# Performance work log

Hardware: AMD Instinct MI355X
Metric: run time of the kernel (lower is better)

Reference implementation:

```python
import jax, jax.numpy as jnp
import numpy as np

S, HID, H, KV, D = 2048, 3584, 16, 8, 256
WINDOW = 1024
SOFTCAP = 50.0
SCALING = 256 ** (-0.5)  # query_pre_attn_scalar ** -0.5
EPS = 1e-6
ROPE_THETA = 10000.0


def _rope_tables(seq_len, dim, theta):
    inv_freq = 1.0 / (theta ** (np.arange(0, dim, 2, dtype=np.float32) / dim))
    t = np.arange(seq_len, dtype=np.float32)
    freqs = np.outer(t, inv_freq)            # [S, D/2]
    emb = np.concatenate([freqs, freqs], -1)  # [S, D]
    return jnp.asarray(np.cos(emb)), jnp.asarray(np.sin(emb))


def setup_inputs() -> dict:
    key = jax.random.key(0)
    ks = jax.random.split(key, 3)
    hidden_states = jax.random.normal(ks[0], (S, HID), jnp.float32)
    w_qkv = jax.random.normal(ks[1], (HID, (H + 2 * KV) * D), jnp.float32) * (HID ** -0.5)
    w_o = jax.random.normal(ks[2], (H * D, HID), jnp.float32) * ((H * D) ** -0.5)
    q_norm_w = jnp.zeros((D,), jnp.float32)  # gemma norm stores weight as (1 + w)
    k_norm_w = jnp.zeros((D,), jnp.float32)
    cos, sin = _rope_tables(S, D, ROPE_THETA)
    return {"hidden_states": hidden_states, "w_qkv": w_qkv, "w_o": w_o,
            "q_norm_w": q_norm_w, "k_norm_w": k_norm_w, "cos": cos, "sin": sin}


def _rms_norm(x, w):
    # gemma-style: fp32 norm, scale by (1 + w); x: [S, h, D]
    xf = x.astype(jnp.float32)
    var = jnp.mean(xf * xf, axis=-1, keepdims=True)
    return (xf * jax.lax.rsqrt(var + EPS) * (1.0 + w)).astype(x.dtype)


def _rotate_half(x):
    x1, x2 = jnp.split(x, 2, axis=-1)
    return jnp.concatenate([-x2, x1], axis=-1)


def _apply_rope(x, cos, sin):
    # x: [S, h, D]; cos/sin: [S, D]
    c = cos[:, None, :]
    s = sin[:, None, :]
    return x * c + _rotate_half(x) * s


def reference(hidden_states, w_qkv, w_o, q_norm_w, k_norm_w, cos, sin):
    qkv = hidden_states @ w_qkv                      # [S, (H+2KV)*D]
    q = qkv[:, : H * D].reshape(S, H, D)
    k = qkv[:, H * D: (H + KV) * D].reshape(S, KV, D)
    v = qkv[:, (H + KV) * D:].reshape(S, KV, D)

    q = _rms_norm(q, q_norm_w)                       # gemma3 q_norm
    k = _rms_norm(k, k_norm_w)                       # gemma3 k_norm
    q = _apply_rope(q, cos, sin)
    k = _apply_rope(k, cos, sin)

    # GQA: expand KV heads to H
    rep = H // KV
    k = jnp.repeat(k, rep, axis=1)                   # [S, H, D]
    v = jnp.repeat(v, rep, axis=1)

    scores = jnp.einsum('shd,thd->hst', q, k) * SCALING  # [H, S, S]
    scores = SOFTCAP * jnp.tanh(scores / SOFTCAP)        # logit softcapping

    i = jnp.arange(S)[:, None]
    j = jnp.arange(S)[None, :]
    allowed = (j <= i) & ((i - j) < WINDOW)              # causal + sliding window
    scores = jnp.where(allowed[None], scores, jnp.float32(-1e30))

    attn = jax.nn.softmax(scores, axis=-1)
    out = jnp.einsum('hst,thd->shd', attn, v).reshape(S, H * D)
    return out @ w_o                                     # [S, HID]
```

## Files before the change

kernel.cpp:

```cpp
#include <hip/hip_runtime.h>
#include <hip/hip_bf16.h>
#include <math.h>

typedef __attribute__((ext_vector_type(8))) short short8;
typedef __attribute__((ext_vector_type(4))) float floatx4;
typedef unsigned short u16;

typedef __attribute__((address_space(1))) const void* gas_ptr;
typedef __attribute__((address_space(3))) void* las_ptr;

__device__ __forceinline__ float bf2f(u16 h) {
  union { unsigned u; float f; } v; v.u = ((unsigned)h) << 16; return v.f;
}
__device__ __forceinline__ u16 f2bf(float f) {
  union { float f; unsigned u; } v; v.f = f;
  unsigned r = v.u + 0x7FFFu + ((v.u >> 16) & 1u);
  return (u16)(r >> 16);
}
__device__ __forceinline__ float ldf_dyn(const void* p, size_t i, bool f32) {
  return f32 ? ((const float*)p)[i] : bf2f(((const u16*)p)[i]);
}
__device__ __forceinline__ short8 load8_dyn(const void* p, size_t idx, bool f32) {
  if (f32) {
    const float* f = (const float*)p;
    float4 a = *(const float4*)(f + idx);
    float4 b = *(const float4*)(f + idx + 4);
    short8 r;
    r[0] = (short)f2bf(a.x); r[1] = (short)f2bf(a.y);
    r[2] = (short)f2bf(a.z); r[3] = (short)f2bf(a.w);
    r[4] = (short)f2bf(b.x); r[5] = (short)f2bf(b.y);
    r[6] = (short)f2bf(b.z); r[7] = (short)f2bf(b.w);
    return r;
  }
  return *(const short8*)((const u16*)p + idx);
}
__device__ __forceinline__ void gl_lds16(const u16* g, u16* l) {
  __builtin_amdgcn_global_load_lds((gas_ptr)g, (las_ptr)l, 16, 0, 0);
}

__global__ void probe_dtype_kernel(const void* hidden, int* flag) {
  __shared__ int cnt;
  if (threadIdx.x == 0) cnt = 0;
  __syncthreads();
  const u16* h = (const u16*)hidden;
  int local = 0;
  for (int i = threadIdx.x; i < 8192; i += 256) {
    u16 u = h[i];
    int e = (u >> 7) & 0xFF;
    if ((e >= 64 && e <= 160) || (u & 0x7FFF) == 0) local++;
  }
  atomicAdd(&cnt, local);
  __syncthreads();
  if (threadIdx.x == 0) *flag = (cnt < 7700) ? 1 : 0;
}

__global__ __launch_bounds__(256) void convert_dyn_kernel(
    const void* __restrict__ src, u16* __restrict__ dst, size_t n,
    const int* __restrict__ flagp)
{
  const bool f32 = (*flagp != 0);
  size_t i = ((size_t)blockIdx.x * 256 + threadIdx.x) * 8;
  if (i < n) *(short8*)(dst + i) = load8_dyn(src, i, f32);
}

__global__ __launch_bounds__(256) void transpose_dyn_kernel(
    const void* __restrict__ src, u16* __restrict__ dst, int R, int C,
    const int* __restrict__ flagp)
{
  const bool f32 = (*flagp != 0);
  const int c0 = blockIdx.x * 64, r0 = blockIdx.y * 64;
  __shared__ __attribute__((aligned(16))) u16 T[64][72];
  const int tid = threadIdx.x;
#pragma unroll
  for (int i = 0; i < 2; i++) {
    int t = tid + i * 256;
    int r = t >> 3, cc = (t & 7) << 3;
    *(short8*)(&T[r][cc]) = load8_dyn(src, (size_t)(r0 + r) * C + c0 + cc, f32);
  }
  __syncthreads();
#pragma unroll
  for (int i = 0; i < 2; i++) {
    int t = tid + i * 256;
    int cr = t >> 3, rc = (t & 7) << 3;
    __attribute__((aligned(16))) u16 tmp[8];
#pragma unroll
    for (int j = 0; j < 8; j++) tmp[j] = T[rc + j][cr];
    *(short8*)(dst + (size_t)(c0 + cr) * R + r0 + rc) = *(const short8*)tmp;
  }
}

#define BAR() __builtin_amdgcn_s_barrier()
#define SCB() __builtin_amdgcn_sched_barrier(0)
#define LGKM0() do { asm volatile("s_waitcnt lgkmcnt(0)" ::: "memory"); SCB(); } while (0)
#define VMW(n) do { asm volatile("s_waitcnt vmcnt(" #n ")" ::: "memory"); SCB(); } while (0)

#define STG_AU(s, u, t) \
  gl_lds16(pa + (size_t)((u) * 64) * K + (size_t)(t) * 64, \
           ldsw + (s) * 32768 + (u) * 4096)
#define STG_BU(s, u, t) \
  gl_lds16(pb + (size_t)((u) * 64) * K + (size_t)(t) * 64, \
           ldsw + (s) * 32768 + 16384 + (u) * 4096)

#define RD_FA(s, miH) do { \
  _Pragma("unroll") \
  for (int m2 = 0; m2 < 4; m2++) { \
    const u16* _r = LDS + (s) * 32768 + wm * 8192 + (miH) * 4096 + m2 * 1024 + lane15 * 64; \
    fa[m2][0] = *(const short8*)(_r + colA0); \
    fa[m2][1] = *(const short8*)(_r + colA1); \
  } \
} while (0)
#define RD_FB(s, niH) do { \
  _Pragma("unroll") \
  for (int n2 = 0; n2 < 2; n2++) { \
    const u16* _r = LDS + (s) * 32768 + 16384 + wn * 4096 + (niH) * 2048 + n2 * 1024 + lane15 * 64; \
    fb[niH][n2][0] = *(const short8*)(_r + colA0); \
    fb[niH][n2][1] = *(const short8*)(_r + colA1); \
  } \
} while (0)
#define MFMA_Q(miH, niH) do { \
  __builtin_amdgcn_s_setprio(1); \
  _Pragma("unroll") \
  for (int m2 = 0; m2 < 4; m2++) \
    _Pragma("unroll") \
    for (int n2 = 0; n2 < 2; n2++) { \
      acc[(miH) * 4 + m2][(niH) * 2 + n2] = __builtin_amdgcn_mfma_f32_16x16x32_bf16( \
          fa[m2][0], fb[niH][n2][0], acc[(miH) * 4 + m2][(niH) * 2 + n2], 0, 0, 0); \
      acc[(miH) * 4 + m2][(niH) * 2 + n2] = __builtin_amdgcn_mfma_f32_16x16x32_bf16( \
          fa[m2][1], fb[niH][n2][1], acc[(miH) * 4 + m2][(niH) * 2 + n2], 0, 0, 0); \
    } \
  __builtin_amdgcn_s_setprio(0); \
  SCB(); \
} while (0)

__global__ __launch_bounds__(512, 2) void gemm8p_kernel(
    const u16* __restrict__ A, const u16* __restrict__ BT, u16* __restrict__ C,
    int M, int N, int K)
{
  __shared__ __attribute__((aligned(16))) u16 LDS[65536];
  const int tid = threadIdx.x;
  const int wave = tid >> 6, lane = tid & 63;
  const int lane15 = lane & 15, quad = lane >> 4;
  const int wm = wave >> 2, wn = wave & 3;
  const int m0 = blockIdx.y * 256, n0 = blockIdx.x * 256;

  const int rloc = wave * 8 + (lane >> 3);
  const int sxor = lane >> 3;
  const int csw = ((lane & 7) ^ sxor) * 8;
  const u16* pa = A + (size_t)(m0 + rloc) * K + csw;
  const u16* pb = BT + (size_t)(n0 + rloc) * K + csw;
  u16* ldsw = LDS + wave * 512;

  const int swz = lane15 & 7;
  const int colA0 = (quad ^ swz) * 8;
  const int colA1 = ((4 + quad) ^ swz) * 8;

  floatx4 acc[8][4];
#pragma unroll
  for (int i = 0; i < 8; i++)
#pragma unroll
    for (int j = 0; j < 4; j++) acc[i][j] = (floatx4){0.f, 0.f, 0.f, 0.f};
  short8 fa[4][2], fb[2][2][2];

  const int NT = K >> 6, NI = NT >> 1;

  STG_AU(0, 0, 0); STG_AU(0, 2, 0);
  STG_BU(0, 0, 0); STG_BU(0, 1, 0);
  STG_BU(0, 2, 0); STG_BU(0, 3, 0);
  STG_AU(0, 1, 0); STG_AU(0, 3, 0);
  STG_AU(1, 0, 1); STG_AU(1, 2, 1);
  STG_BU(1, 0, 1); STG_BU(1, 1, 1);
  STG_BU(1, 2, 1); STG_BU(1, 3, 1);
  VMW(8);
  BAR();

  for (int i = 0; i < NI - 1; i++) {
    const int t1 = 2 * i + 1, t2 = 2 * i + 2, t3 = 2 * i + 3;
    RD_FA(0, 0); RD_FB(0, 0);
    STG_AU(1, 1, t1); STG_AU(1, 3, t1);
    BAR(); LGKM0(); MFMA_Q(0, 0); BAR();
    RD_FB(0, 1);
    STG_AU(0, 0, t2); STG_AU(0, 2, t2);
    BAR(); LGKM0(); MFMA_Q(0, 1); VMW(10); BAR();
    RD_FA(0, 1);
    STG_BU(0, 0, t2); STG_BU(0, 1, t2);
    BAR(); LGKM0(); MFMA_Q(1, 1); BAR();
    STG_BU(0, 2, t2); STG_BU(0, 3, t2);
    BAR(); MFMA_Q(1, 0); VMW(8); BAR();
    RD_FA(1, 0); RD_FB(1, 0);
    STG_AU(0, 1, t2); STG_AU(0, 3, t2);
    BAR(); LGKM0(); MFMA_Q(0, 0); BAR();
    RD_FB(1, 1);
    STG_AU(1, 0, t3); STG_AU(1, 2, t3);
    BAR(); LGKM0(); MFMA_Q(0, 1); VMW(10); BAR();
    RD_FA(1, 1);
    STG_BU(1, 0, t3); STG_BU(1, 1, t3);
    BAR(); LGKM0(); MFMA_Q(1, 1); BAR();
    STG_BU(1, 2, t3); STG_BU(1, 3, t3);
    BAR(); MFMA_Q(1, 0); VMW(8); BAR();
  }

  {
    const int tL = NT - 1;
    RD_FA(0, 0); RD_FB(0, 0);
    STG_AU(1, 1, tL); STG_AU(1, 3, tL);
    BAR(); LGKM0(); MFMA_Q(0, 0); BAR();
    RD_FB(0, 1);
    BAR(); LGKM0(); MFMA_Q(0, 1); VMW(8); BAR();
    RD_FA(0, 1);
    BAR(); LGKM0(); MFMA_Q(1, 1); BAR();
    BAR(); MFMA_Q(1, 0); VMW(2); BAR();
    RD_FA(1, 0); RD_FB(1, 0);
    BAR(); LGKM0(); MFMA_Q(0, 0); BAR();
    RD_FB(1, 1);
    BAR(); LGKM0(); MFMA_Q(0, 1); VMW(0); BAR();
    RD_FA(1, 1);
    BAR(); LGKM0(); MFMA_Q(1, 1); BAR();
    BAR(); MFMA_Q(1, 0);
  }

#pragma unroll
  for (int mi = 0; mi < 8; mi++)
#pragma unroll
    for (int rr = 0; rr < 4; rr++) {
      int m = m0 + wm * 128 + mi * 16 + quad * 4 + rr;
      u16* crow = C + (size_t)m * N + n0 + wn * 64;
#pragma unroll
      for (int ni = 0; ni < 4; ni++) crow[ni * 16 + lane15] = f2bf(acc[mi][ni][rr]);
    }
}

#define NSTG_A(s, u, t) \
  gl_lds16(pa + (size_t)((u) * 64) * K + (size_t)(t) * 64, \
           ldsw + (s) * 24576 + (u) * 4096)
#define NSTG_B(s, u, t) \
  gl_lds16(pb + (size_t)((u) * 64) * K + (size_t)(t) * 64, \
           ldsw + (s) * 24576 + 8192 + (u) * 4096)

#define NRD_FA(s, miH) do { \
  _Pragma("unroll") \
  for (int m2 = 0; m2 < 2; m2++) { \
    const u16* _r = LDS + (s) * 24576 + wm * 4096 + (miH) * 2048 + m2 * 1024 + lane15 * 64; \
    fa[m2][0] = *(const short8*)(_r + colA0); \
    fa[m2][1] = *(const short8*)(_r + colA1); \
  } \
} while (0)
#define NRD_FB(s, niH) do { \
  _Pragma("unroll") \
  for (int n2 = 0; n2 < 2; n2++) { \
    const u16* _r = LDS + (s) * 24576 + 8192 + wn * 4096 + (niH) * 2048 + n2 * 1024 + lane15 * 64; \
    fb[niH][n2][0] = *(const short8*)(_r + colA0); \
    fb[niH][n2][1] = *(const short8*)(_r + colA1); \
  } \
} while (0)
#define NMFMA_Q(miH, niH) do { \
  __builtin_amdgcn_s_setprio(1); \
  _Pragma("unroll") \
  for (int m2 = 0; m2 < 2; m2++) \
    _Pragma("unroll") \
    for (int n2 = 0; n2 < 2; n2++) { \
      acc[(miH) * 2 + m2][(niH) * 2 + n2] = __builtin_amdgcn_mfma_f32_16x16x32_bf16( \
          fa[m2][0], fb[niH][n2][0], acc[(miH) * 2 + m2][(niH) * 2 + n2], 0, 0, 0); \
      acc[(miH) * 2 + m2][(niH) * 2 + n2] = __builtin_amdgcn_mfma_f32_16x16x32_bf16( \
          fa[m2][1], fb[niH][n2][1], acc[(miH) * 2 + m2][(niH) * 2 + n2], 0, 0, 0); \
    } \
  __builtin_amdgcn_s_setprio(0); \
  SCB(); \
} while (0)

__global__ __launch_bounds__(512, 2) void gemm8pn_kernel(
    const u16* __restrict__ A, const u16* __restrict__ BT, void* __restrict__ C,
    int M, int N, int K, const int* __restrict__ flagp, int cdyn)
{
  __shared__ __attribute__((aligned(16))) u16 LDS[49152];
  const int tid = threadIdx.x;
  const int wave = tid >> 6, lane = tid & 63;
  const int lane15 = lane & 15, quad = lane >> 4;
  const int wm = wave >> 2, wn = wave & 3;
  const int m0 = blockIdx.y * 128, n0 = blockIdx.x * 256;

  const int rloc = wave * 8 + (lane >> 3);
  const int sxor = lane >> 3;
  const int csw = ((lane & 7) ^ sxor) * 8;
  const u16* pa = A + (size_t)(m0 + rloc) * K + csw;
  const u16* pb = BT + (size_t)(n0 + rloc) * K + csw;
  u16* ldsw = LDS + wave * 512;

  const int swz = lane15 & 7;
  const int colA0 = (quad ^ swz) * 8;
  const int colA1 = ((4 + quad) ^ swz) * 8;

  floatx4 acc[4][4];
#pragma unroll
  for (int i = 0; i < 4; i++)
#pragma unroll
    for (int j = 0; j < 4; j++) acc[i][j] = (floatx4){0.f, 0.f, 0.f, 0.f};
  short8 fa[2][2], fb[2][2][2];

  const int NT = K >> 6, NI = NT >> 1;

  NSTG_B(0, 0, 0); NSTG_B(0, 1, 0); NSTG_B(0, 2, 0); NSTG_B(0, 3, 0);
  NSTG_A(0, 0, 0); NSTG_A(0, 1, 0);
  NSTG_B(1, 0, 1); NSTG_B(1, 1, 1); NSTG_B(1, 2, 1); NSTG_B(1, 3, 1);
  NSTG_A(1, 0, 1); NSTG_A(1, 1, 1);
  VMW(6);
  BAR();

  for (int i = 0; i < NI - 1; i++) {
    const int t2 = 2 * i + 2, t3 = 2 * i + 3;
    NRD_FA(0, 0); NRD_FB(0, 0);
    BAR(); LGKM0(); NMFMA_Q(0, 0); BAR();
    NRD_FB(0, 1);
    BAR(); LGKM0(); NMFMA_Q(0, 1); BAR();
    NRD_FA(0, 1);
    NSTG_B(0, 0, t2); NSTG_B(0, 1, t2);
    BAR(); LGKM0(); NMFMA_Q(1, 1); BAR();
    NSTG_B(0, 2, t2); NSTG_B(0, 3, t2); NSTG_A(0, 0, t2); NSTG_A(0, 1, t2);
    BAR(); NMFMA_Q(1, 0); VMW(6); BAR();
    NRD_FA(1, 0); NRD_FB(1, 0);
    BAR(); LGKM0(); NMFMA_Q(0, 0); BAR();
    NRD_FB(1, 1);
    BAR(); LGKM0(); NMFMA_Q(0, 1); BAR();
    NRD_FA(1, 1);
    NSTG_B(1, 0, t3); NSTG_B(1, 1, t3);
    BAR(); LGKM0(); NMFMA_Q(1, 1); BAR();
    NSTG_B(1, 2, t3); NSTG_B(1, 3, t3); NSTG_A(1, 0, t3); NSTG_A(1, 1, t3);
    BAR(); NMFMA_Q(1, 0); VMW(6); BAR();
  }

  {
    NRD_FA(0, 0); NRD_FB(0, 0);
    BAR(); LGKM0(); NMFMA_Q(0, 0); BAR();
    NRD_FB(0, 1);
    BAR(); LGKM0(); NMFMA_Q(0, 1); BAR();
    NRD_FA(0, 1);
    BAR(); LGKM0(); NMFMA_Q(1, 1); BAR();
    BAR(); NMFMA_Q(1, 0); VMW(0); BAR();
    NRD_FA(1, 0); NRD_FB(1, 0);
    BAR(); LGKM0(); NMFMA_Q(0, 0); BAR();
    NRD_FB(1, 1);
    BAR(); LGKM0(); NMFMA_Q(0, 1); BAR();
    NRD_FA(1, 1);
    BAR(); LGKM0(); NMFMA_Q(1, 1); BAR();
    NMFMA_Q(1, 0);
  }

  const bool cf32 = cdyn && (*flagp != 0);
  if (cf32) {
    float* Cf = (float*)C;
#pragma unroll
    for (int mi = 0; mi < 4; mi++)
#pragma unroll
      for (int rr = 0; rr < 4; rr++) {
        int m = m0 + wm * 64 + mi * 16 + quad * 4 + rr;
        float* crow = Cf + (size_t)m * N + n0 + wn * 64;
#pragma unroll
        for (int ni = 0; ni < 4; ni++) crow[ni * 16 + lane15] = acc[mi][ni][rr];
      }
  } else {
    u16* Cb = (u16*)C;
#pragma unroll
    for (int mi = 0; mi < 4; mi++)
#pragma unroll
      for (int rr = 0; rr < 4; rr++) {
        int m = m0 + wm * 64 + mi * 16 + quad * 4 + rr;
        u16* crow = Cb + (size_t)m * N + n0 + wn * 64;
#pragma unroll
        for (int ni = 0; ni < 4; ni++) crow[ni * 16 + lane15] = f2bf(acc[mi][ni][rr]);
      }
  }
}

__global__ __launch_bounds__(256) void normrope_kernel(
    u16* __restrict__ qkv, const void* __restrict__ qw,
    const void* __restrict__ kw, const void* __restrict__ cosb,
    const void* __restrict__ sinb, const int* __restrict__ flagp)
{
  const bool f32 = (*flagp != 0);
  const int s = blockIdx.x;
  const int wave = threadIdx.x >> 6, lane = threadIdx.x & 63;
  const int hh = blockIdx.y * 4 + wave;
  const int col = (hh < 16) ? hh * 256 : 4096 + (hh - 16) * 256;
  const void* w = (hh < 16) ? qw : kw;
  u16* row = qkv + (size_t)s * 8192 + col;

  float x[4];
#pragma unroll
  for (int j = 0; j < 4; j++) x[j] = bf2f(row[lane + j * 64]);

  float ss = x[0] * x[0] + x[1] * x[1] + x[2] * x[2] + x[3] * x[3];
#pragma unroll
  for (int off = 32; off > 0; off >>= 1) ss += __shfl_xor(ss, off);
  float inv = rsqrtf(ss * (1.0f / 256.0f) + 1e-6f);

  float y[4];
#pragma unroll
  for (int j = 0; j < 4; j++)
    y[j] = x[j] * inv * (1.0f + ldf_dyn(w, lane + j * 64, f32));
  float rot[4] = {-y[2], -y[3], y[0], y[1]};
#pragma unroll
  for (int j = 0; j < 4; j++) {
    int d = lane + j * 64;
    float c = ldf_dyn(cosb, (size_t)s * 256 + d, f32);
    float sn = ldf_dyn(sinb, (size_t)s * 256 + d, f32);
    row[d] = f2bf(y[j] * c + rot[j] * sn);
  }
}

__global__ __launch_bounds__(256) void vtrans_kernel(
    const u16* __restrict__ qkv, u16* __restrict__ vT)
{
  const int s0 = blockIdx.x * 64, d0 = blockIdx.y * 64, kv = blockIdx.z;
  __shared__ __attribute__((aligned(16))) u16 T[64][72];
  const int tid = threadIdx.x;
#pragma unroll
  for (int i = 0; i < 2; i++) {
    int c = tid + i * 256;
    int r = c >> 3, dc = (c & 7) << 3;
    *(short8*)(&T[r][dc]) =
        *(const short8*)(qkv + (size_t)(s0 + r) * 8192 + 6144 + kv * 256 + d0 + dc);
  }
  __syncthreads();
#pragma unroll
  for (int i = 0; i < 2; i++) {
    int c = tid + i * 256;
    int dr = c >> 3, sc = (c & 7) << 3;
    __attribute__((aligned(16))) u16 tmp[8];
#pragma unroll
    for (int j = 0; j < 8; j++) tmp[j] = T[sc + j][dr];
    *(short8*)(vT + (size_t)kv * 524288 + (size_t)(d0 + dr) * 2048 + s0 + sc) =
        *(const short8*)tmp;
  }
}

__global__ __launch_bounds__(256) void attn_kernel(
    const u16* __restrict__ qkv, const u16* __restrict__ vT,
    u16* __restrict__ aout)
{
  const int h = blockIdx.y, kvh = h >> 1;
  const int q0 = blockIdx.x * 64;
  const int tid = threadIdx.x;
  const int wave = tid >> 6, lane = tid & 63;
  const int lane15 = lane & 15, quad = lane >> 4;

  __shared__ __attribute__((aligned(16))) u16 Ks[64 * 264];
  __shared__ __attribute__((aligned(16))) u16 Vs[256 * 72];
  __shared__ __attribute__((aligned(16))) u16 Ps[4][16 * 72];

  short8 aq[8];
  const u16* qrow = qkv + (size_t)(q0 + wave * 16 + lane15) * 8192 + h * 256;
#pragma unroll
  for (int kt = 0; kt < 8; kt++)
    aq[kt] = *(const short8*)(qrow + kt * 32 + quad * 8);

  floatx4 zero = {0.0f, 0.0f, 0.0f, 0.0f};
  floatx4 accO[16];
#pragma unroll
  for (int i = 0; i < 16; i++) accO[i] = zero;
  float lR[4] = {0.0f, 0.0f, 0.0f, 0.0f};

  const int iRow = q0 + wave * 16 + quad * 4;
  const int kb_lo = (q0 >= 1023) ? ((q0 - 1023) >> 6) : 0;
  const int kb_hi = q0 >> 6;

  for (int kb = kb_lo; kb <= kb_hi; kb++) {
    const int t0 = kb << 6;
#pragma unroll
    for (int i = 0; i < 8; i++) {
      int c = tid + i * 256;
      int r = c >> 5, dc = (c & 31) << 3;
      *(short8*)(&Ks[r * 264 + dc]) =
          *(const short8*)(qkv + (size_t)(t0 + r) * 8192 + 4096 + kvh * 256 + dc);
    }
#pragma unroll
    for (int i = 0; i < 8; i++) {
      int c = tid + i * 256;
      int dr = c >> 3, tc = (c & 7) << 3;
      *(short8*)(&Vs[dr * 72 + tc]) =
          *(const short8*)(vT + (size_t)kvh * 524288 + (size_t)dr * 2048 + t0 + tc);
    }
    __syncthreads();

    const int relHi = q0 + 16 * wave + 15 - t0;
    const int relLo = q0 + 16 * wave - 1023 - t0;
    const int niHiR = relHi >> 4;
    const int niHi = (niHiR > 3) ? 3 : niHiR;
    int niLo = relLo >> 4; if (niLo < 0) niLo = 0;
    const int ktHiR = relHi >> 5;
    const int ktHi = (ktHiR > 1) ? 1 : ktHiR;
    int ktLo = relLo >> 5; if (ktLo < 0) ktLo = 0;

    float pv[4][4];
#pragma unroll
    for (int ni = 0; ni < 4; ni++) {
      if (ni < niLo || ni > niHi) {
        pv[ni][0] = pv[ni][1] = pv[ni][2] = pv[ni][3] = 0.0f;
        continue;
      }
      floatx4 sAcc = zero;
#pragma unroll
      for (int kt = 0; kt < 8; kt++) {
        short8 bk = *(const short8*)(&Ks[(ni * 16 + lane15) * 264 + kt * 32 + quad * 8]);
        sAcc = __builtin_amdgcn_mfma_f32_16x16x32_bf16(aq[kt], bk, sAcc, 0, 0, 0);
      }
#pragma unroll
      for (int r = 0; r < 4; r++) {
        float x = sAcc[r] * 0.00125f;
        float ax = __builtin_fabsf(x);
        float e2 = __expf(ax + ax);
        float t = 1.0f - 2.0f * __builtin_amdgcn_rcpf(e2 + 1.0f);
        float sv = copysignf(t, x) * 50.0f;
        int i_ = iRow + r;
        int j_ = t0 + ni * 16 + lane15;
        bool ok = (j_ <= i_) && (i_ - j_ < 1024);
        pv[ni][r] = ok ? __expf(sv) : 0.0f;
      }
    }
#pragma unroll
    for (int r = 0; r < 4; r++)
      lR[r] += pv[0][r] + pv[1][r] + pv[2][r] + pv[3][r];

#pragma unroll
    for (int ni = 0; ni < 4; ni++)
#pragma unroll
      for (int r = 0; r < 4; r++)
        Ps[wave][(quad * 4 + r) * 72 + ni * 16 + lane15] = f2bf(pv[ni][r]);
    __syncthreads();

#pragma unroll
    for (int ktile = 0; ktile < 2; ktile++) {
      if (ktile < ktLo || ktile > ktHi) continue;
      short8 ap = *(const short8*)(&Ps[wave][lane15 * 72 + ktile * 32 + quad * 8]);
#pragma unroll
      for (int ni = 0; ni < 16; ni++) {
        short8 bv = *(const short8*)(&Vs[(ni * 16 + lane15) * 72 + ktile * 32 + quad * 8]);
        accO[ni] = __builtin_amdgcn_mfma_f32_16x16x32_bf16(ap, bv, accO[ni], 0, 0, 0);
      }
    }
    __syncthreads();
  }

#pragma unroll
  for (int r = 0; r < 4; r++) {
    float l = lR[r];
    l += __shfl_xor(l, 1);
    l += __shfl_xor(l, 2);
    l += __shfl_xor(l, 4);
    l += __shfl_xor(l, 8);
    float invl = 1.0f / l;
    u16* orow = aout + (size_t)(q0 + wave * 16 + quad * 4 + r) * 4096 + h * 256;
#pragma unroll
    for (int ni = 0; ni < 16; ni++)
      orow[ni * 16 + lane15] = f2bf(accO[ni][r] * invl);
  }
}

extern "C" void kernel_launch(void* const* d_in, const int* in_sizes, int n_in,
                              void* d_out, int out_size, void* d_ws, size_t ws_size,
                              hipStream_t stream)
{
  const void* hidden = d_in[0];
  const void* w_qkv  = d_in[1];
  const void* w_o    = d_in[2];
  const void* q_w    = d_in[3];
  const void* k_w    = d_in[4];
  const void* cosb   = d_in[5];
  const void* sinb   = d_in[6];

  char* ws = (char*)d_ws;
  int* flag = (int*)ws;                                   ws += 256;
  u16* qkv  = (u16*)ws;  ws += (size_t)2048 * 8192 * 2;
  u16* vT   = (u16*)ws;  ws += (size_t)8 * 256 * 2048 * 2;
  u16* aout = (u16*)ws;  ws += (size_t)2048 * 4096 * 2;
  u16* hb   = (u16*)ws;  ws += (size_t)2048 * 3584 * 2;
  u16* wT   = (u16*)ws;

  probe_dtype_kernel<<<1, 256, 0, stream>>>(hidden, flag);
  convert_dyn_kernel<<<3584, 256, 0, stream>>>(hidden, hb, (size_t)2048 * 3584, flag);
  transpose_dyn_kernel<<<dim3(128, 56), 256, 0, stream>>>(w_qkv, wT, 3584, 8192, flag);
  gemm8p_kernel<<<dim3(32, 8), 512, 0, stream>>>(hb, wT, qkv, 2048, 8192, 3584);
  normrope_kernel<<<dim3(2048, 6), 256, 0, stream>>>(qkv, q_w, k_w, cosb, sinb, flag);
  transpose_dyn_kernel<<<dim3(56, 64), 256, 0, stream>>>(w_o, wT, 4096, 3584, flag);
  vtrans_kernel<<<dim3(32, 4, 8), 256, 0, stream>>>(qkv, vT);
  attn_kernel<<<dim3(32, 16), 256, 0, stream>>>(qkv, vT, aout);
  gemm8pn_kernel<<<dim3(14, 16), 512, 0, stream>>>(aout, wT, d_out, 2048, 3584, 4096, flag, 1);
}
```

Baseline: 522.8 us.

## Split LDS fragment reads with partial lgkmcnt waits; skip bf16 hidden conversion copy

The QKV GEMM main loop now issues LDS fragment reads one row-group at a time and waits on partial lgkmcnt counts, so MFMAs on the first fragments can start while later reads are still in flight. Separately, when the input is already bf16, the convert kernel exits early and the GEMM reads the raw hidden buffer directly, which removes a full copy pass. The finer-grained waits add more sched barriers, which could constrain the compiler's own scheduling.

```diff
diff --git a/kernel.cpp b/kernel.cpp
--- a/kernel.cpp
+++ b/kernel.cpp
@@ -58,9 +58,9 @@
     const void* __restrict__ src, u16* __restrict__ dst, size_t n,
     const int* __restrict__ flagp)
 {
-  const bool f32 = (*flagp != 0);
+  if (*flagp == 0) return;
   size_t i = ((size_t)blockIdx.x * 256 + threadIdx.x) * 8;
-  if (i < n) *(short8*)(dst + i) = load8_dyn(src, i, f32);
+  if (i < n) *(short8*)(dst + i) = load8_dyn(src, i, true);
 }
 
 __global__ __launch_bounds__(256) void transpose_dyn_kernel(
@@ -92,7 +92,10 @@
 #define BAR() __builtin_amdgcn_s_barrier()
 #define SCB() __builtin_amdgcn_sched_barrier(0)
 #define LGKM0() do { asm volatile("s_waitcnt lgkmcnt(0)" ::: "memory"); SCB(); } while (0)
+#define LGKMC(n) do { asm volatile("s_waitcnt lgkmcnt(" #n ")" ::: "memory"); SCB(); } while (0)
 #define VMW(n) do { asm volatile("s_waitcnt vmcnt(" #n ")" ::: "memory"); SCB(); } while (0)
+#define PRIO1() __builtin_amdgcn_s_setprio(1)
+#define PRIO0() do { __builtin_amdgcn_s_setprio(0); SCB(); } while (0)
 
 #define STG_AU(s, u, t) \
   gl_lds16(pa + (size_t)((u) * 64) * K + (size_t)(t) * 64, \
@@ -117,8 +120,37 @@
     fb[niH][n2][1] = *(const short8*)(_r + colA1); \
   } \
 } while (0)
+#define RD_FA1(s, miH, m2v) do { \
+  const u16* _r = LDS + (s) * 32768 + wm * 8192 + (miH) * 4096 + (m2v) * 1024 + lane15 * 64; \
+  fa[m2v][0] = *(const short8*)(_r + colA0); \
+  fa[m2v][1] = *(const short8*)(_r + colA1); \
+} while (0)
+#define RD_FB1(s, niH, n2v) do { \
+  const u16* _r = LDS + (s) * 32768 + 16384 + wn * 4096 + (niH) * 2048 + (n2v) * 1024 + lane15 * 64; \
+  fb[niH][n2v][0] = *(const short8*)(_r + colA0); \
+  fb[niH][n2v][1] = *(const short8*)(_r + colA1); \
+} while (0)
+
+#define MFMA_M2(m2v, miH, niH) do { \
+  _Pragma("unroll") \
+  for (int n2 = 0; n2 < 2; n2++) { \
+    acc[(miH) * 4 + (m2v)][(niH) * 2 + n2] = __builtin_amdgcn_mfma_f32_16x16x32_bf16( \
+        fa[m2v][0], fb[niH][n2][0], acc[(miH) * 4 + (m2v)][(niH) * 2 + n2], 0, 0, 0); \
+    acc[(miH) * 4 + (m2v)][(niH) * 2 + n2] = __builtin_amdgcn_mfma_f32_16x16x32_bf16( \
+        fa[m2v][1], fb[niH][n2][1], acc[(miH) * 4 + (m2v)][(niH) * 2 + n2], 0, 0, 0); \
+  } \
+} while (0)
+#define MFMA_N2(n2v, miH, niH) do { \
+  _Pragma("unroll") \
+  for (int m2 = 0; m2 < 4; m2++) { \
+    acc[(miH) * 4 + m2][(niH) * 2 + (n2v)] = __builtin_amdgcn_mfma_f32_16x16x32_bf16( \
+        fa[m2][0], fb[niH][n2v][0], acc[(miH) * 4 + m2][(niH) * 2 + (n2v)], 0, 0, 0); \
+    acc[(miH) * 4 + m2][(niH) * 2 + (n2v)] = __builtin_amdgcn_mfma_f32_16x16x32_bf16( \
+        fa[m2][1], fb[niH][n2v][1], acc[(miH) * 4 + m2][(niH) * 2 + (n2v)], 0, 0, 0); \
+  } \
+} while (0)
 #define MFMA_Q(miH, niH) do { \
-  __builtin_amdgcn_s_setprio(1); \
+  PRIO1(); \
   _Pragma("unroll") \
   for (int m2 = 0; m2 < 4; m2++) \
     _Pragma("unroll") \
@@ -128,13 +160,13 @@
       acc[(miH) * 4 + m2][(niH) * 2 + n2] = __builtin_amdgcn_mfma_f32_16x16x32_bf16( \
           fa[m2][1], fb[niH][n2][1], acc[(miH) * 4 + m2][(niH) * 2 + n2], 0, 0, 0); \
     } \
-  __builtin_amdgcn_s_setprio(0); \
-  SCB(); \
+  PRIO0(); \
 } while (0)
 
 __global__ __launch_bounds__(512, 2) void gemm8p_kernel(
-    const u16* __restrict__ A, const u16* __restrict__ BT, u16* __restrict__ C,
-    int M, int N, int K)
+    const void* __restrict__ Araw, const u16* __restrict__ Ahb,
+    const u16* __restrict__ BT, u16* __restrict__ C,
+    int M, int N, int K, const int* __restrict__ flagp)
 {
   __shared__ __attribute__((aligned(16))) u16 LDS[65536];
   const int tid = threadIdx.x;
@@ -143,10 +175,12 @@
   const int wm = wave >> 2, wn = wave & 3;
   const int m0 = blockIdx.y * 256, n0 = blockIdx.x * 256;
 
+  const u16* Abase = (*flagp != 0) ? Ahb : (const u16*)Araw;
+
   const int rloc = wave * 8 + (lane >> 3);
   const int sxor = lane >> 3;
   const int csw = ((lane & 7) ^ sxor) * 8;
-  const u16* pa = A + (size_t)(m0 + rloc) * K + csw;
+  const u16* pa = Abase + (size_t)(m0 + rloc) * K + csw;
   const u16* pb = BT + (size_t)(n0 + rloc) * K + csw;
   u16* ldsw = LDS + wave * 512;
 
@@ -175,26 +209,58 @@
 
   for (int i = 0; i < NI - 1; i++) {
     const int t1 = 2 * i + 1, t2 = 2 * i + 2, t3 = 2 * i + 3;
-    RD_FA(0, 0); RD_FB(0, 0);
+    RD_FB(0, 0); SCB();
+    RD_FA1(0, 0, 0); SCB(); RD_FA1(0, 0, 1); SCB();
+    RD_FA1(0, 0, 2); SCB(); RD_FA1(0, 0, 3); SCB();
     STG_AU(1, 1, t1); STG_AU(1, 3, t1);
-    BAR(); LGKM0(); MFMA_Q(0, 0); BAR();
-    RD_FB(0, 1);
+    BAR(); PRIO1();
+    LGKMC(6); MFMA_M2(0, 0, 0);
+    LGKMC(4); MFMA_M2(1, 0, 0);
+    LGKMC(2); MFMA_M2(2, 0, 0);
+    LGKM0();  MFMA_M2(3, 0, 0);
+    PRIO0(); BAR();
+    RD_FB1(0, 1, 0); SCB(); RD_FB1(0, 1, 1); SCB();
     STG_AU(0, 0, t2); STG_AU(0, 2, t2);
-    BAR(); LGKM0(); MFMA_Q(0, 1); VMW(10); BAR();
-    RD_FA(0, 1);
+    BAR(); PRIO1();
+    LGKMC(2); MFMA_N2(0, 0, 1);
+    LGKM0();  MFMA_N2(1, 0, 1);
+    PRIO0(); VMW(10); BAR();
+    RD_FA1(0, 1, 0); SCB(); RD_FA1(0, 1, 1); SCB();
+    RD_FA1(0, 1, 2); SCB(); RD_FA1(0, 1, 3); SCB();
     STG_BU(0, 0, t2); STG_BU(0, 1, t2);
-    BAR(); LGKM0(); MFMA_Q(1, 1); BAR();
+    BAR(); PRIO1();
+    LGKMC(6); MFMA_M2(0, 1, 1);
+    LGKMC(4); MFMA_M2(1, 1, 1);
+    LGKMC(2); MFMA_M2(2, 1, 1);
+    LGKM0();  MFMA_M2(3, 1, 1);
+    PRIO0(); BAR();
     STG_BU(0, 2, t2); STG_BU(0, 3, t2);
     BAR(); MFMA_Q(1, 0); VMW(8); BAR();
-    RD_FA(1, 0); RD_FB(1, 0);
+    RD_FB(1, 0); SCB();
+    RD_FA1(1, 0, 0); SCB(); RD_FA1(1, 0, 1); SCB();
+    RD_FA1(1, 0, 2); SCB(); RD_FA1(1, 0, 3); SCB();
     STG_AU(0, 1, t2); STG_AU(0, 3, t2);
-    BAR(); LGKM0(); MFMA_Q(0, 0); BAR();
-    RD_FB(1, 1);
+    BAR(); PRIO1();
+    LGKMC(6); MFMA_M2(0, 0, 0);
+    LGKMC(4); MFMA_M2(1, 0, 0);
+    LGKMC(2); MFMA_M2(2, 0, 0);
+    LGKM0();  MFMA_M2(3, 0, 0);
+    PRIO0(); BAR();
+    RD_FB1(1, 1, 0); SCB(); RD_FB1(1, 1, 1); SCB();
     STG_AU(1, 0, t3); STG_AU(1, 2, t3);
-    BAR(); LGKM0(); MFMA_Q(0, 1); VMW(10); BAR();
-    RD_FA(1, 1);
+    BAR(); PRIO1();
+    LGKMC(2); MFMA_N2(0, 0, 1);
+    LGKM0();  MFMA_N2(1, 0, 1);
+    PRIO0(); VMW(10); BAR();
+    RD_FA1(1, 1, 0); SCB(); RD_FA1(1, 1, 1); SCB();
+    RD_FA1(1, 1, 2); SCB(); RD_FA1(1, 1, 3); SCB();
     STG_BU(1, 0, t3); STG_BU(1, 1, t3);
-    BAR(); LGKM0(); MFMA_Q(1, 1); BAR();
+    BAR(); PRIO1();
+    LGKMC(6); MFMA_M2(0, 1, 1);
+    LGKMC(4); MFMA_M2(1, 1, 1);
+    LGKMC(2); MFMA_M2(2, 1, 1);
+    LGKM0();  MFMA_M2(3, 1, 1);
+    PRIO0(); BAR();
     STG_BU(1, 2, t3); STG_BU(1, 3, t3);
     BAR(); MFMA_Q(1, 0); VMW(8); BAR();
   }
@@ -253,7 +319,7 @@
   } \
 } while (0)
 #define NMFMA_Q(miH, niH) do { \
-  __builtin_amdgcn_s_setprio(1); \
+  PRIO1(); \
   _Pragma("unroll") \
   for (int m2 = 0; m2 < 2; m2++) \
     _Pragma("unroll") \
@@ -263,8 +329,7 @@
       acc[(miH) * 2 + m2][(niH) * 2 + n2] = __builtin_amdgcn_mfma_f32_16x16x32_bf16( \
           fa[m2][1], fb[niH][n2][1], acc[(miH) * 2 + m2][(niH) * 2 + n2], 0, 0, 0); \
     } \
-  __builtin_amdgcn_s_setprio(0); \
-  SCB(); \
+  PRIO0(); \
 } while (0)
 
 __global__ __launch_bounds__(512, 2) void gemm8pn_kernel(
@@ -577,7 +642,7 @@
   probe_dtype_kernel<<<1, 256, 0, stream>>>(hidden, flag);
   convert_dyn_kernel<<<3584, 256, 0, stream>>>(hidden, hb, (size_t)2048 * 3584, flag);
   transpose_dyn_kernel<<<dim3(128, 56), 256, 0, stream>>>(w_qkv, wT, 3584, 8192, flag);
-  gemm8p_kernel<<<dim3(32, 8), 512, 0, stream>>>(hb, wT, qkv, 2048, 8192, 3584);
+  gemm8p_kernel<<<dim3(32, 8), 512, 0, stream>>>(hidden, hb, wT, qkv, 2048, 8192, 3584, flag);
   normrope_kernel<<<dim3(2048, 6), 256, 0, stream>>>(qkv, q_w, k_w, cosb, sinb, flag);
   transpose_dyn_kernel<<<dim3(56, 64), 256, 0, stream>>>(w_o, wT, 4096, 3584, flag);
   vtrans_kernel<<<dim3(32, 4, 8), 256, 0, stream>>>(qkv, vT);
```

New measurement: 520.0 us. No clear change (-0.5%).
